# Optimization experiments

Hardware: AMD Instinct MI355X
Metric: run time of the kernel (lower is better)

## Reference

```python
import jax, jax.numpy as jnp
import numpy as np

HIDDEN = 1024
RANK = 4
INPUT = 16
ALPHA = 0.1
BASE_SCALE = 500.0
B = 32
T = 1024


def setup_inputs() -> dict:
    key = jax.random.key(0)
    k1, k2, k3, k4 = jax.random.split(key, 4)
    std = HIDDEN ** -0.25  # matches cov ~ I/sqrt(hidden) in original init
    x = jax.random.normal(k1, (B, T, INPUT), dtype=jnp.float32)
    m = jax.random.normal(k2, (HIDDEN, RANK), dtype=jnp.float32) * std
    n = jax.random.normal(k3, (HIDDEN, RANK), dtype=jnp.float32) * std
    I_mat = jax.random.normal(k4, (HIDDEN, INPUT), dtype=jnp.float32) * std
    return {"x": x, "m": m, "n": n, "I_mat": I_mat}


def reference(x, m, n, I_mat):
    # J = (m @ n.T) * base_scale / hidden ; recurrent term (J @ tanh(h).T).T
    # == tanh(h) @ J.T == ((tanh(h) @ n) @ m.T) * scale  (low-rank form, same math)
    scale = BASE_SCALE / HIDDEN

    def step(h, x_t):
        rec = (jnp.tanh(h) @ n) @ m.T * scale          # [B, H]
        dh = -h + rec + x_t @ I_mat.T                  # [B, H]
        h = h + ALPHA * dh
        return h, h

    h0 = jnp.zeros((x.shape[0], HIDDEN), dtype=x.dtype)
    _, hiddens = jax.lax.scan(step, h0, jnp.swapaxes(x, 0, 1))  # [T, B, H]
    hiddens = jnp.swapaxes(hiddens, 0, 1)                       # [B, T, H]

    span = jnp.concatenate([m, I_mat], axis=1)   # [H, RANK+INPUT]
    proj = jnp.linalg.pinv(span)                 # [RANK+INPUT, H]
    # (pinv(span) @ hiddens.permute(0,2,1)).permute(0,2,1)
    return jnp.einsum('ph,bth->btp', proj, hiddens)  # [B, T, RANK+INPUT]
```

## Files before the change

### kernel.cpp

```cpp
#include <hip/hip_runtime.h>
#include <math.h>

#define HIDDEN_ 1024
#define RANK_ 4
#define INPUT_ 16
#define T_ 1024
#define BATCH_ 32

#define SCAN_THREADS_ 512
#define NW_ (SCAN_THREADS_ / 64)
#define EPT_ (HIDDEN_ / SCAN_THREADS_)
#define CH_ 64
#define NCH_ (T_ / CH_)

#define FTPB_ 256
#define FEPT_ 4
#define FNW_ 4

#define PRE_BLOCKS_ 2048
#define ROWS_ (BATCH_ * T_)
#define PASSES_ (ROWS_ / PRE_BLOCKS_)

typedef float f32x4 __attribute__((ext_vector_type(4)));

__device__ __forceinline__ float fast_exp2(float x) {
#if defined(__has_builtin)
#if __has_builtin(__builtin_amdgcn_exp2f)
    return __builtin_amdgcn_exp2f(x);
#else
    return exp2f(x);
#endif
#else
    return exp2f(x);
#endif
}

__device__ __forceinline__ float fast_rcp(float x) {
#if defined(__has_builtin)
#if __has_builtin(__builtin_amdgcn_rcpf)
    return __builtin_amdgcn_rcpf(x);
#else
    return 1.0f / x;
#endif
#else
    return 1.0f / x;
#endif
}

__device__ __forceinline__ float tanh_fast(float x) {
    float e = fast_exp2(x * 2.885390081777926815f);
    return fmaf(-2.0f, fast_rcp(e + 1.0f), 1.0f);
}

#define DPP_ADD(v, ctrl)                                                          \
    do {                                                                          \
        int _t = __builtin_amdgcn_update_dpp(0, __float_as_int(v), (ctrl), 0xf,   \
                                             0xf, true);                          \
        (v) += __int_as_float(_t);                                                \
    } while (0)

__global__ __launch_bounds__(FTPB_, 2) void precompute_u(
    const float* __restrict__ x,
    const float* __restrict__ imat,
    float* __restrict__ u)
{
    const int tid = threadIdx.x;
    const int bid = blockIdx.x;
    const float kin = 0.1f;

    float Ir[4][INPUT_];
#pragma unroll
    for (int r = 0; r < 4; ++r) {
        const float* ip = imat + (4 * tid + r) * INPUT_;
#pragma unroll
        for (int q = 0; q < 4; ++q) {
            const float4 v = *(const float4*)(ip + 4 * q);
            Ir[r][q*4+0] = kin * v.x; Ir[r][q*4+1] = kin * v.y;
            Ir[r][q*4+2] = kin * v.z; Ir[r][q*4+3] = kin * v.w;
        }
    }

    for (int p = 0; p < PASSES_; ++p) {
        const int row = p * PRE_BLOCKS_ + bid;
        const float* xr = x + (size_t)row * INPUT_;
        float xv[INPUT_];
#pragma unroll
        for (int q = 0; q < 4; ++q) {
            const float4 v = ((const float4*)xr)[q];
            xv[q*4+0] = v.x; xv[q*4+1] = v.y; xv[q*4+2] = v.z; xv[q*4+3] = v.w;
        }
        float4 acc;
        float a[4];
#pragma unroll
        for (int r = 0; r < 4; ++r) {
            float s0 = xv[0] * Ir[r][0];
            float s1 = xv[1] * Ir[r][1];
#pragma unroll
            for (int i = 2; i < INPUT_; i += 2) {
                s0 = fmaf(xv[i],     Ir[r][i],     s0);
                s1 = fmaf(xv[i + 1], Ir[r][i + 1], s1);
            }
            a[r] = s0 + s1;
        }
        acc.x = a[0]; acc.y = a[1]; acc.z = a[2]; acc.w = a[3];
        *(float4*)(u + (size_t)row * HIDDEN_ + 4 * tid) = acc;
    }
}

__global__ __launch_bounds__(SCAN_THREADS_)
__attribute__((amdgpu_waves_per_eu(2, 2)))
void rnn_scan_kernel(
    const float* __restrict__ x,
    const float* __restrict__ m,
    const float* __restrict__ n,
    const float* __restrict__ u,
    float* __restrict__ out)
{
    const int tid  = threadIdx.x;
    const int wv   = tid >> 6;
    const int lane = tid & 63;
    const int b    = blockIdx.x;

    const float kd   = 0.9f;
    const float krec = 0.1f * (500.0f / 1024.0f);

    float h[EPT_];
    float mrs[EPT_][RANK_];
    float nr[EPT_][RANK_];
#pragma unroll
    for (int j = 0; j < EPT_; ++j) {
        const int hidx = tid * EPT_ + j;
        h[j] = 0.0f;
        const float4 mv = *(const float4*)(m + hidx * RANK_);
        mrs[j][0] = krec * mv.x; mrs[j][1] = krec * mv.y;
        mrs[j][2] = krec * mv.z; mrs[j][3] = krec * mv.w;
        const float4 nv = *(const float4*)(n + hidx * RANK_);
        nr[j][0] = nv.x; nr[j][1] = nv.y; nr[j][2] = nv.z; nr[j][3] = nv.w;
    }

    __shared__ float4 part[2][NW_];
    __shared__ float xs[2][CH_ * INPUT_];

    const float* xb = x + (size_t)b * T_ * INPUT_;
    const float* ub = u + (size_t)b * T_ * HIDDEN_ + tid * EPT_;
    float* ob = out + (size_t)b * T_ * (RANK_ + INPUT_);

    float4 xstage = make_float4(0.f, 0.f, 0.f, 0.f);
    if (tid < 256) {
        float4 c0 = *(const float4*)(xb + tid * 4);
        *(float4*)&xs[0][tid * 4] = c0;
        xstage = *(const float4*)(xb + CH_ * INPUT_ + tid * 4);
    }

    float2 upf[4];
#pragma unroll
    for (int k = 0; k < 4; ++k)
        upf[k] = *(const float2*)(ub + (size_t)k * HIDDEN_);

    float y = 0.0f;
    const int yoff = (tid >= 4 && tid < 20) ? (tid - 4) : 0;

#pragma unroll 4
    for (int t = 0; t < T_; ++t) {
        float th[EPT_];
#pragma unroll
        for (int j = 0; j < EPT_; ++j) th[j] = tanh_fast(h[j]);

        float p0 = th[0] * nr[0][0], p1 = th[0] * nr[0][1];
        float p2 = th[0] * nr[0][2], p3 = th[0] * nr[0][3];
#pragma unroll
        for (int j = 1; j < EPT_; ++j) {
            p0 = fmaf(th[j], nr[j][0], p0);
            p1 = fmaf(th[j], nr[j][1], p1);
            p2 = fmaf(th[j], nr[j][2], p2);
            p3 = fmaf(th[j], nr[j][3], p3);
        }

        DPP_ADD(p0, 0x111); DPP_ADD(p1, 0x111); DPP_ADD(p2, 0x111); DPP_ADD(p3, 0x111);
        DPP_ADD(p0, 0x112); DPP_ADD(p1, 0x112); DPP_ADD(p2, 0x112); DPP_ADD(p3, 0x112);
        DPP_ADD(p0, 0x114); DPP_ADD(p1, 0x114); DPP_ADD(p2, 0x114); DPP_ADD(p3, 0x114);
        DPP_ADD(p0, 0x118); DPP_ADD(p1, 0x118); DPP_ADD(p2, 0x118); DPP_ADD(p3, 0x118);
        DPP_ADD(p0, 0x142); DPP_ADD(p1, 0x142); DPP_ADD(p2, 0x142); DPP_ADD(p3, 0x142);
        DPP_ADD(p0, 0x143); DPP_ADD(p1, 0x143); DPP_ADD(p2, 0x143); DPP_ADD(p3, 0x143);

        if (lane == 63) part[t & 1][wv] = make_float4(p0, p1, p2, p3);

        asm volatile("s_waitcnt lgkmcnt(0)\n\ts_barrier" ::: "memory");

        if ((t & (CH_ - 1)) == 0) {
            if (tid < 256) {
                const int c = t >> 6;
                *(float4*)&xs[(c + 1) & 1][tid * 4] = xstage;
                const int cl = (c + 2 < NCH_) ? (c + 2) : (NCH_ - 1);
                xstage = *(const float4*)(xb + cl * CH_ * INPUT_ + tid * 4);
            }
        }

        const float4 a0 = part[t & 1][0];
        const float4 a1 = part[t & 1][1];
        const float4 a2 = part[t & 1][2];
        const float4 a3 = part[t & 1][3];
        const float4 a4 = part[t & 1][4];
        const float4 a5 = part[t & 1][5];
        const float4 a6 = part[t & 1][6];
        const float4 a7 = part[t & 1][7];
        const float xyv = xs[(t >> 6) & 1][(t & 63) * INPUT_ + yoff];

        const float2 uv = upf[t & 3];
        {
            const int tn = (t + 4 < T_) ? (t + 4) : t;
            upf[t & 3] = *(const float2*)(ub + (size_t)tn * HIDDEN_);
        }

        const float4 sv4 = ((a0 + a1) + (a2 + a3)) + ((a4 + a5) + (a6 + a7));
        const float s0 = sv4.x, s1 = sv4.y, s2 = sv4.z, s3 = sv4.w;

        const float uq[2] = {uv.x, uv.y};
#pragma unroll
        for (int j = 0; j < EPT_; ++j) {
            float a01 = fmaf(s1, mrs[j][1], fmaf(s0, mrs[j][0], uq[j]));
            float a23 = fmaf(s3, mrs[j][3], s2 * mrs[j][2]);
            h[j] = fmaf(kd, h[j], a01 + a23);
        }

        if (tid < 20) {
            float drive;
            if (tid < 4) {
                float sv = (tid == 0) ? s0 : (tid == 1) ? s1 : (tid == 2) ? s2 : s3;
                drive = krec * sv;
            } else {
                drive = 0.1f * xyv;
            }
            y = fmaf(kd, y, drive);
            ob[t * 20 + tid] = y;
        }
    }
}

__global__ __launch_bounds__(FTPB_)
__attribute__((amdgpu_waves_per_eu(1, 1)))
void rnn_scan_fallback(
    const float* __restrict__ x, const float* __restrict__ m,
    const float* __restrict__ n, const float* __restrict__ imat,
    float* __restrict__ out)
{
    const int b    = blockIdx.x;
    const int tid  = threadIdx.x;
    const int wave = tid >> 6;
    const int lane = tid & 63;
    const float kd = 0.9f, krec = 0.1f * (500.0f / 1024.0f), kin = 0.1f;

    float h[FEPT_], mrs[FEPT_][RANK_], nr[FEPT_][RANK_], Irs[FEPT_][INPUT_];
#pragma unroll
    for (int j = 0; j < FEPT_; ++j) {
        const int hidx = tid * FEPT_ + j;
        h[j] = 0.0f;
        const float4 mv = *(const float4*)(m + hidx * RANK_);
        mrs[j][0] = krec * mv.x; mrs[j][1] = krec * mv.y;
        mrs[j][2] = krec * mv.z; mrs[j][3] = krec * mv.w;
        const float4 nv = *(const float4*)(n + hidx * RANK_);
        nr[j][0] = nv.x; nr[j][1] = nv.y; nr[j][2] = nv.z; nr[j][3] = nv.w;
#pragma unroll
        for (int q = 0; q < 4; ++q) {
            const float4 iv = *(const float4*)(imat + hidx * INPUT_ + q * 4);
            Irs[j][q*4+0] = kin * iv.x; Irs[j][q*4+1] = kin * iv.y;
            Irs[j][q*4+2] = kin * iv.z; Irs[j][q*4+3] = kin * iv.w;
        }
    }
    __shared__ float4 part[2][FNW_];
    __shared__ float xs[2][CH_ * INPUT_];
    const float* xb = x + (size_t)b * T_ * INPUT_;
    float* ob = out + (size_t)b * T_ * (RANK_ + INPUT_);
    {
        float4 c0 = *(const float4*)(xb + tid * 4);
        *(float4*)&xs[0][tid * 4] = c0;
    }
    float4 xstage = *(const float4*)(xb + CH_ * INPUT_ + tid * 4);
    float y = 0.0f;
    const int yoff = (tid >= 4 && tid < 20) ? (tid - 4) : 0;

    for (int t = 0; t < T_; ++t) {
        float th[FEPT_];
#pragma unroll
        for (int j = 0; j < FEPT_; ++j) th[j] = tanh_fast(h[j]);
        float p0 = th[0] * nr[0][0], p1 = th[0] * nr[0][1];
        float p2 = th[0] * nr[0][2], p3 = th[0] * nr[0][3];
#pragma unroll
        for (int j = 1; j < FEPT_; ++j) {
            p0 = fmaf(th[j], nr[j][0], p0); p1 = fmaf(th[j], nr[j][1], p1);
            p2 = fmaf(th[j], nr[j][2], p2); p3 = fmaf(th[j], nr[j][3], p3);
        }
        DPP_ADD(p0, 0x111); DPP_ADD(p1, 0x111); DPP_ADD(p2, 0x111); DPP_ADD(p3, 0x111);
        DPP_ADD(p0, 0x112); DPP_ADD(p1, 0x112); DPP_ADD(p2, 0x112); DPP_ADD(p3, 0x112);
        DPP_ADD(p0, 0x114); DPP_ADD(p1, 0x114); DPP_ADD(p2, 0x114); DPP_ADD(p3, 0x114);
        DPP_ADD(p0, 0x118); DPP_ADD(p1, 0x118); DPP_ADD(p2, 0x118); DPP_ADD(p3, 0x118);
        DPP_ADD(p0, 0x142); DPP_ADD(p1, 0x142); DPP_ADD(p2, 0x142); DPP_ADD(p3, 0x142);
        DPP_ADD(p0, 0x143); DPP_ADD(p1, 0x143); DPP_ADD(p2, 0x143); DPP_ADD(p3, 0x143);
        if (lane == 63) part[t & 1][wave] = make_float4(p0, p1, p2, p3);
        asm volatile("s_waitcnt lgkmcnt(0)\n\ts_barrier" ::: "memory");
        if ((t & (CH_ - 1)) == 0) {
            const int c = t >> 6;
            *(float4*)&xs[(c + 1) & 1][tid * 4] = xstage;
            const int cl = (c + 2 < NCH_) ? (c + 2) : (NCH_ - 1);
            xstage = *(const float4*)(xb + cl * CH_ * INPUT_ + tid * 4);
        }
        const float* xsp = &xs[(t >> 6) & 1][(t & 63) * INPUT_];
        const float4 xa = ((const float4*)xsp)[0];
        const float4 xbv = ((const float4*)xsp)[1];
        const float4 xc = ((const float4*)xsp)[2];
        const float4 xd = ((const float4*)xsp)[3];
        const float xyv = xsp[yoff];
        const float4 q0 = part[t & 1][0];
        const float4 q1 = part[t & 1][1];
        const float4 q2 = part[t & 1][2];
        const float4 q3 = part[t & 1][3];
        float ax[FEPT_];
#pragma unroll
        for (int j = 0; j < FEPT_; ++j) {
            float a = xa.x * Irs[j][0];
            float c = xa.y * Irs[j][1];
            a = fmaf(xa.z, Irs[j][2], a);   c = fmaf(xa.w, Irs[j][3], c);
            a = fmaf(xbv.x, Irs[j][4], a);  c = fmaf(xbv.y, Irs[j][5], c);
            a = fmaf(xbv.z, Irs[j][6], a);  c = fmaf(xbv.w, Irs[j][7], c);
            a = fmaf(xc.x, Irs[j][8], a);   c = fmaf(xc.y, Irs[j][9], c);
            a = fmaf(xc.z, Irs[j][10], a);  c = fmaf(xc.w, Irs[j][11], c);
            a = fmaf(xd.x, Irs[j][12], a);  c = fmaf(xd.y, Irs[j][13], c);
            a = fmaf(xd.z, Irs[j][14], a);  c = fmaf(xd.w, Irs[j][15], c);
            ax[j] = a + c;
        }
        const float s0 = (q0.x + q1.x) + (q2.x + q3.x);
        const float s1 = (q0.y + q1.y) + (q2.y + q3.y);
        const float s2 = (q0.z + q1.z) + (q2.z + q3.z);
        const float s3 = (q0.w + q1.w) + (q2.w + q3.w);
#pragma unroll
        for (int j = 0; j < FEPT_; ++j) {
            float a01 = fmaf(s1, mrs[j][1], fmaf(s0, mrs[j][0], ax[j]));
            float a23 = fmaf(s3, mrs[j][3], s2 * mrs[j][2]);
            h[j] = fmaf(kd, h[j], a01 + a23);
        }
        if (tid < 20) {
            float drive;
            if (tid < 4) {
                float sv = (tid == 0) ? s0 : (tid == 1) ? s1 : (tid == 2) ? s2 : s3;
                drive = krec * sv;
            } else {
                drive = kin * xyv;
            }
            y = fmaf(kd, y, drive);
            ob[t * 20 + tid] = y;
        }
    }
}

extern "C" void kernel_launch(void* const* d_in, const int* in_sizes, int n_in,
                              void* d_out, int out_size, void* d_ws, size_t ws_size,
                              hipStream_t stream) {
    const float* x    = (const float*)d_in[0];
    const float* m    = (const float*)d_in[1];
    const float* n    = (const float*)d_in[2];
    const float* imat = (const float*)d_in[3];
    float* out = (float*)d_out;

    const size_t u_bytes = (size_t)BATCH_ * T_ * HIDDEN_ * sizeof(float);
    if (d_ws != nullptr && ws_size >= u_bytes) {
        float* u = (float*)d_ws;
        precompute_u<<<dim3(PRE_BLOCKS_), dim3(FTPB_), 0, stream>>>(x, imat, u);
        rnn_scan_kernel<<<dim3(BATCH_), dim3(SCAN_THREADS_), 0, stream>>>(x, m, n, u, out);
    } else {
        rnn_scan_fallback<<<dim3(BATCH_), dim3(FTPB_), 0, stream>>>(x, m, n, imat, out);
    }
}
```

Before: 573.9 us.

## Stage input drive through LDS in chunks and batch output writes via shared buffer

New measurement: 572.1 us. Within noise of the previous version (-0.3%).

```diff
diff --git a/kernel.cpp b/kernel.cpp
--- a/kernel.cpp
+++ b/kernel.cpp
@@ -12,6 +12,8 @@
 #define EPT_ (HIDDEN_ / SCAN_THREADS_)
 #define CH_ 64
 #define NCH_ (T_ / CH_)
+#define UCH_ 4
+#define NUCH_ (T_ / UCH_)
 
 #define FTPB_ 256
 #define FEPT_ 4
@@ -20,8 +22,6 @@
 #define PRE_BLOCKS_ 2048
 #define ROWS_ (BATCH_ * T_)
 #define PASSES_ (ROWS_ / PRE_BLOCKS_)
-
-typedef float f32x4 __attribute__((ext_vector_type(4)));
 
 __device__ __forceinline__ float fast_exp2(float x) {
 #if defined(__has_builtin)
@@ -140,9 +140,11 @@
 
     __shared__ float4 part[2][NW_];
     __shared__ float xs[2][CH_ * INPUT_];
-
-    const float* xb = x + (size_t)b * T_ * INPUT_;
-    const float* ub = u + (size_t)b * T_ * HIDDEN_ + tid * EPT_;
+    __shared__ float us[2][UCH_ * HIDDEN_];
+    __shared__ float ys[2][CH_ * 20];
+
+    const float* xb  = x + (size_t)b * T_ * INPUT_;
+    const float* ub0 = u + (size_t)b * T_ * HIDDEN_;
     float* ob = out + (size_t)b * T_ * (RANK_ + INPUT_);
 
     float4 xstage = make_float4(0.f, 0.f, 0.f, 0.f);
@@ -151,11 +153,16 @@
         *(float4*)&xs[0][tid * 4] = c0;
         xstage = *(const float4*)(xb + CH_ * INPUT_ + tid * 4);
     }
-
-    float2 upf[4];
-#pragma unroll
-    for (int k = 0; k < 4; ++k)
-        upf[k] = *(const float2*)(ub + (size_t)k * HIDDEN_);
+    {
+        float4 a0 = *(const float4*)(ub0 + tid * 8);
+        float4 a1 = *(const float4*)(ub0 + tid * 8 + 4);
+        *(float4*)&us[0][tid * 8]     = a0;
+        *(float4*)&us[0][tid * 8 + 4] = a1;
+    }
+    float4 ust0 = *(const float4*)(ub0 + UCH_ * HIDDEN_ + tid * 8);
+    float4 ust1 = *(const float4*)(ub0 + UCH_ * HIDDEN_ + tid * 8 + 4);
+
+    __syncthreads();
 
     float y = 0.0f;
     const int yoff = (tid >= 4 && tid < 20) ? (tid - 4) : 0;
@@ -187,12 +194,30 @@
 
         asm volatile("s_waitcnt lgkmcnt(0)\n\ts_barrier" ::: "memory");
 
+        if ((t & (UCH_ - 1)) == 0) {
+            const int c = t >> 2;
+            float* du = &us[(c + 1) & 1][0];
+            *(float4*)&du[tid * 8]     = ust0;
+            *(float4*)&du[tid * 8 + 4] = ust1;
+            const int cl = (c + 2 < NUCH_) ? (c + 2) : (NUCH_ - 1);
+            ust0 = *(const float4*)(ub0 + (size_t)cl * UCH_ * HIDDEN_ + tid * 8);
+            ust1 = *(const float4*)(ub0 + (size_t)cl * UCH_ * HIDDEN_ + tid * 8 + 4);
+        }
+
         if ((t & (CH_ - 1)) == 0) {
             if (tid < 256) {
                 const int c = t >> 6;
                 *(float4*)&xs[(c + 1) & 1][tid * 4] = xstage;
                 const int cl = (c + 2 < NCH_) ? (c + 2) : (NCH_ - 1);
                 xstage = *(const float4*)(xb + cl * CH_ * INPUT_ + tid * 4);
+            }
+            if (t != 0) {
+                const int tc = (t >> 6) - 1;
+                const float* src = &ys[tc & 1][0];
+                float* dst = ob + (size_t)tc * (CH_ * 20);
+                dst[tid]       = src[tid];
+                dst[tid + 512] = src[tid + 512];
+                if (tid < 256) dst[tid + 1024] = src[tid + 1024];
             }
         }
 
@@ -205,12 +230,7 @@
         const float4 a6 = part[t & 1][6];
         const float4 a7 = part[t & 1][7];
         const float xyv = xs[(t >> 6) & 1][(t & 63) * INPUT_ + yoff];
-
-        const float2 uv = upf[t & 3];
-        {
-            const int tn = (t + 4 < T_) ? (t + 4) : t;
-            upf[t & 3] = *(const float2*)(ub + (size_t)tn * HIDDEN_);
-        }
+        const float2 uv = *(const float2*)&us[(t >> 2) & 1][(t & 3) * HIDDEN_ + tid * EPT_];
 
         const float4 sv4 = ((a0 + a1) + (a2 + a3)) + ((a4 + a5) + (a6 + a7));
         const float s0 = sv4.x, s1 = sv4.y, s2 = sv4.z, s3 = sv4.w;
@@ -232,8 +252,18 @@
                 drive = 0.1f * xyv;
             }
             y = fmaf(kd, y, drive);
-            ob[t * 20 + tid] = y;
-        }
+            ys[(t >> 6) & 1][(t & 63) * 20 + tid] = y;
+        }
+    }
+
+    asm volatile("s_waitcnt lgkmcnt(0)\n\ts_barrier" ::: "memory");
+    {
+        const int tc = NCH_ - 1;
+        const float* src = &ys[tc & 1][0];
+        float* dst = ob + (size_t)tc * (CH_ * 20);
+        dst[tid]       = src[tid];
+        dst[tid + 512] = src[tid + 512];
+        if (tid < 256) dst[tid + 1024] = src[tid + 1024];
     }
 }
 
```
